# Kernel tuning notes

Measured on AMD Instinct MI355X. Metric: run time of the kernel, lower is better.

Reference implementation:

```python
import jax, jax.numpy as jnp
import numpy as np

N, F, H, R, B, L, C, E, NB = 8192, 512, 256, 16, 32, 256, 7, 262144, 30
D = F + H


def setup_inputs() -> dict:
    ks = jax.random.split(jax.random.key(0), 16)
    g = lambda k, shape, fan: jax.random.normal(k, shape, jnp.float32) / np.sqrt(fan)
    return {
        "x": jax.random.normal(ks[0], (N, F), jnp.float32),
        "edge_index": jax.random.randint(ks[1], (2, E), 0, N),
        "edge_norm": jax.random.uniform(ks[2], (E,), jnp.float32),
        "edge_type": jax.random.randint(ks[3], (E,), 0, R),
        "seq_lengths": jnp.full((B,), L, dtype=jnp.int32),
        "umask": jnp.ones((B, L), jnp.float32),
        "nodal_attn": 1,
        "avec": 0,
        "basis": g(ks[4], (NB, F, H), F),
        "comp": g(ks[5], (R, NB), NB),
        "root1": g(ks[6], (F, H), F),
        "bias1": jnp.zeros((H,), jnp.float32),
        "w_rel": g(ks[7], (H, H), H),
        "b_rel": jnp.zeros((H,), jnp.float32),
        "w_root": g(ks[8], (H, H), H),
        "w_att": g(ks[9], (D, D), D),
        "b_att": jnp.zeros((D,), jnp.float32),
        "w_lin": g(ks[10], (D, H), D),
        "b_lin": jnp.zeros((H,), jnp.float32),
        "w_fc": g(ks[11], (H, C), H),
        "b_fc": jnp.zeros((C,), jnp.float32),
    }


def reference(x, edge_index, edge_norm, edge_type, seq_lengths, umask,
              nodal_attn, avec, basis, comp, root1, bias1, w_rel, b_rel,
              w_root, w_att, b_att, w_lin, b_lin, w_fc, b_fc):
    n = x.shape[0]
    r = comp.shape[0]
    src, dst = edge_index[0], edge_index[1]
    # ---- RGCNConv (num_bases basis decomposition, mean aggregation per relation, root + bias)
    W = jnp.einsum('rb,bfh->rfh', comp, basis)             # [R,F,H]
    xw = jnp.einsum('nf,rfh->nrh', x, W)                   # [N,R,H]
    msg = xw[src, edge_type]                               # [E,H] gather per edge
    seg = dst * r + edge_type                              # per (node, relation) segment
    cnt = jax.ops.segment_sum(jnp.ones((msg.shape[0],), msg.dtype), seg, num_segments=n * r)
    msg = msg / jnp.maximum(cnt[seg], 1.0)[:, None]
    out1 = jax.ops.segment_sum(msg, dst, num_segments=n) + x @ root1 + bias1
    # ---- GraphConv (add aggregation): W_rel * sum_j h_j + b_rel + W_root * h_i
    agg2 = jax.ops.segment_sum(out1[src], dst, num_segments=n)
    out2 = agg2 @ w_rel + b_rel + out1 @ w_root
    emotions = jnp.concatenate([x, out2], axis=-1)          # [N, F+H]
    if int(nodal_attn):
        seq = np.asarray(seq_lengths)                       # static conversation lengths
        starts = np.concatenate([[0], np.cumsum(seq)[:-1]])
        lmax = int(seq.max())
        rows = [jnp.pad(jax.lax.dynamic_slice_in_dim(emotions, int(s), int(l)),
                        ((0, lmax - int(l)), (0, 0)))
                for s, l in zip(starts, seq)]
        M = jnp.stack(rows, 0).transpose(1, 0, 2)           # [L, B, D]
        mask = umask                                        # [B, L]
        # MatchingAttention 'general2', vectorized over all timesteps t
        X = M @ w_att + b_att                               # transform(x_t) for every t: [L,B,D]
        Mm = M * mask.T[:, :, None]                         # mask memory over seq dim
        scores = jnp.einsum('tbd,sbd->tbs', X, Mm) * mask[None]
        a = jax.nn.softmax(jnp.tanh(scores), axis=-1) * mask[None]
        a = a / jnp.sum(a, axis=-1, keepdims=True)
        att = jnp.einsum('tbs,sbd->tbd', a, M)              # [L,B,D]
        hidden = jax.nn.relu(att @ w_lin + b_lin)
    else:
        hidden = jax.nn.relu(emotions @ w_lin + b_lin)
    # dropout is identity in eval mode
    logits = hidden @ w_fc + b_fc
    if int(avec):
        return logits
    return jax.nn.log_softmax(logits, axis=1)  # faithful: torch uses dim=1
```

## Files before the change

kernel.cpp:

```cpp
#include <hip/hip_runtime.h>
#include <hip/hip_bf16.h>

#define NN 8192
#define FF 512
#define HH 256
#define RR 16
#define BB 32
#define LL 256
#define CC 7
#define EE 262144
#define NBASE 30
#define DD 768

constexpr int FLAG_BIAS = 1, FLAG_RELU = 4, FLAG_TANH = 8,
              FLAG_SPLITOUT = 16, FLAG_TAILOUT = 32, FLAG_TAIL2 = 64;

typedef __attribute__((ext_vector_type(8))) short bf16x8;
typedef __attribute__((ext_vector_type(4))) float f32x4;

__global__ __launch_bounds__(256) void detect_dtype(const unsigned short* __restrict__ xs,
                                                    int* __restrict__ flag) {
  __shared__ int red[256];
  int cnt = 0;
  for (int i = threadIdx.x * 2; i < 8192; i += 512) {
    unsigned short u = xs[i];
    int e = (u >> 7) & 0xFF;
    if (e >= 0xC0) cnt++;
  }
  red[threadIdx.x] = cnt;
  __syncthreads();
  for (int s = 128; s > 0; s >>= 1) {
    if (threadIdx.x < s) red[threadIdx.x] += red[threadIdx.x + s];
    __syncthreads();
  }
  if (threadIdx.x == 0) flag[0] = (red[0] > 16) ? 1 : 0;
}

struct PSeg {
  const void* src;
  float* dst;
  __hip_bfloat16* hi;
  __hip_bfloat16* lo;
  __hip_bfloat16* hi2;
  __hip_bfloat16* lo2;
  long n;
  int R, C, ld, off;
  int type;
  int zero;
};
struct PTable {
  PSeg seg[16];
  int count;
  long total;
};

__global__ __launch_bounds__(256) void prep_all(PTable t, const int* __restrict__ flag) {
  const int fp32 = flag[0];
  for (long i = (long)blockIdx.x * 256 + threadIdx.x; i < t.total;
       i += (long)gridDim.x * 256) {
    long off = i;
    int s = 0;
    while (off >= t.seg[s].n) { off -= t.seg[s].n; s++; }
    const PSeg& sg = t.seg[s];
    if (sg.type == 0) {
      float v = 0.f;
      if (!sg.zero)
        v = fp32 ? ((const float*)sg.src)[off]
                 : __bfloat162float(((const __hip_bfloat16*)sg.src)[off]);
      if (sg.dst) sg.dst[off] = v;
      if (sg.hi) {
        __hip_bfloat16 h = __float2bfloat16(v);
        __hip_bfloat16 l = __float2bfloat16(v - __bfloat162float(h));
        sg.hi[off] = h;
        sg.lo[off] = l;
        if (sg.hi2) {
          long d2 = (off >> 9) * DD + (off & 511);
          sg.hi2[d2] = h;
          sg.lo2[d2] = l;
        }
      }
    } else {
      int r = (int)(off % sg.R), c = (int)(off / sg.R);
      float v = fp32 ? ((const float*)sg.src)[(long)r * sg.C + c]
                     : __bfloat162float(((const __hip_bfloat16*)sg.src)[(long)r * sg.C + c]);
      __hip_bfloat16 h = __float2bfloat16(v);
      long d = (long)c * sg.ld + sg.off + r;
      sg.hi[d] = h;
      sg.lo[d] = __float2bfloat16(v - __bfloat162float(h));
    }
  }
}

__global__ __launch_bounds__(256) void wt_gemm(
    const float* __restrict__ basis, const float* __restrict__ comp,
    float* __restrict__ wt_nat) {
  __shared__ float cs[RR * NBASE];
  int tid = threadIdx.x;
  for (int i = tid; i < RR * NBASE; i += 256) cs[i] = comp[i];
  __syncthreads();
  long col = (long)blockIdx.x * 256 + tid;
  float acc[RR] = {};
  for (int b = 0; b < NBASE; ++b) {
    float v = basis[(long)b * 131072 + col];
#pragma unroll
    for (int r = 0; r < RR; ++r) acc[r] += cs[r * NBASE + b] * v;
  }
#pragma unroll
  for (int r = 0; r < RR; ++r) wt_nat[(long)r * 131072 + col] = acc[r];
}

__global__ __launch_bounds__(256) void wt_transpose(
    const float* __restrict__ wt_nat,
    __hip_bfloat16* __restrict__ hi, __hip_bfloat16* __restrict__ lo) {
  __shared__ float t[32][33];
  const int r = blockIdx.z;
  const int f0 = blockIdx.y * 32, h0 = blockIdx.x * 32;
  const int c = threadIdx.x & 31, rw = threadIdx.x >> 5;
  const float* src = wt_nat + ((long)r * 512 + f0) * 256 + h0;
#pragma unroll
  for (int i = 0; i < 4; ++i)
    t[rw + i * 8][c] = src[(long)(rw + i * 8) * 256 + c];
  __syncthreads();
#pragma unroll
  for (int i = 0; i < 4; ++i) {
    int hh = rw + i * 8;
    float v = t[c][hh];
    long orow = (long)(r * 256 + h0 + hh) * 512 + f0 + c;
    __hip_bfloat16 hv = __float2bfloat16(v);
    hi[orow] = hv;
    lo[orow] = __float2bfloat16(v - __bfloat162float(hv));
  }
}

__device__ __forceinline__ void gload_lds16(const void* g, void* l) {
  __builtin_amdgcn_global_load_lds(
      (const __attribute__((address_space(1))) unsigned int*)g,
      (__attribute__((address_space(3))) unsigned int*)l, 16, 0, 0);
}

__global__ __launch_bounds__(256, 3) void mfma_dual(
    const __hip_bfloat16* __restrict__ A, const __hip_bfloat16* __restrict__ Alo,
    const __hip_bfloat16* __restrict__ Bt, const __hip_bfloat16* __restrict__ Btlo,
    const float* __restrict__ bias, float* __restrict__ C, float* __restrict__ Ct,
    __hip_bfloat16* __restrict__ Chi, __hip_bfloat16* __restrict__ Clo,
    __hip_bfloat16* __restrict__ Chi2, __hip_bfloat16* __restrict__ Clo2,
    int K, int ldc, long sA, long sB, long sC, int flags) {
  __shared__ __hip_bfloat16 Ah[128 * 32];
  __shared__ __hip_bfloat16 Bh[128 * 32];
  __shared__ __hip_bfloat16 Al[128 * 32];
  __shared__ __hip_bfloat16 Bl[128 * 32];
  const int tid = threadIdx.x;
  const int w = tid >> 6, lane = tid & 63;
  const long z = blockIdx.z;
  const long row0 = (long)blockIdx.y * 128, col0 = (long)blockIdx.x * 128;
  const int wm = w & 1, wn = w >> 1;
  const int srow0 = (w * 128 + lane) >> 2;
  const int srow1 = (w * 128 + 64 + lane) >> 2;
  const int kch = (lane & 3) * 8;
  const int fr = lane & 15, q = lane >> 4;
  const bool hasAlo = (Alo != nullptr);
  const __hip_bfloat16* Az = A + z * sA;
  const __hip_bfloat16* Alz = hasAlo ? (Alo + z * sA) : nullptr;
  const __hip_bfloat16* Bz = Bt + z * sB;
  const __hip_bfloat16* Blz = Btlo + z * sB;
  const long aoff0 = (row0 + srow0) * K + kch, aoff1 = (row0 + srow1) * K + kch;
  const long boff0 = (col0 + srow0) * K + kch, boff1 = (col0 + srow1) * K + kch;
  f32x4 acc[4][4] = {};
  for (int k0 = 0; k0 < K; k0 += 32) {
    gload_lds16(Az + aoff0 + k0, Ah + w * 1024);
    gload_lds16(Az + aoff1 + k0, Ah + w * 1024 + 512);
    gload_lds16(Bz + boff0 + k0, Bh + w * 1024);
    gload_lds16(Bz + boff1 + k0, Bh + w * 1024 + 512);
    gload_lds16(Blz + boff0 + k0, Bl + w * 1024);
    gload_lds16(Blz + boff1 + k0, Bl + w * 1024 + 512);
    if (hasAlo) {
      gload_lds16(Alz + aoff0 + k0, Al + w * 1024);
      gload_lds16(Alz + aoff1 + k0, Al + w * 1024 + 512);
    }
    __syncthreads();
    bf16x8 ah[4], bh[4], bl[4];
#pragma unroll
    for (int i = 0; i < 4; ++i) {
      ah[i] = *(const bf16x8*)&Ah[(wm * 64 + i * 16 + fr) * 32 + q * 8];
      bh[i] = *(const bf16x8*)&Bh[(wn * 64 + i * 16 + fr) * 32 + q * 8];
      bl[i] = *(const bf16x8*)&Bl[(wn * 64 + i * 16 + fr) * 32 + q * 8];
    }
#pragma unroll
    for (int i = 0; i < 4; ++i)
#pragma unroll
      for (int j = 0; j < 4; ++j) {
        acc[i][j] = __builtin_amdgcn_mfma_f32_16x16x32_bf16(ah[i], bh[j], acc[i][j], 0, 0, 0);
        acc[i][j] = __builtin_amdgcn_mfma_f32_16x16x32_bf16(ah[i], bl[j], acc[i][j], 0, 0, 0);
      }
    if (hasAlo) {
      bf16x8 al[4];
#pragma unroll
      for (int i = 0; i < 4; ++i)
        al[i] = *(const bf16x8*)&Al[(wm * 64 + i * 16 + fr) * 32 + q * 8];
#pragma unroll
      for (int i = 0; i < 4; ++i)
#pragma unroll
        for (int j = 0; j < 4; ++j)
          acc[i][j] = __builtin_amdgcn_mfma_f32_16x16x32_bf16(al[i], bh[j], acc[i][j], 0, 0, 0);
    }
    __syncthreads();
  }
  const int cr = (lane >> 4) * 4, cc = lane & 15;
  float* Cz = C ? (C + z * sC) : nullptr;
  __hip_bfloat16* Chz = Chi ? (Chi + z * sC) : nullptr;
  __hip_bfloat16* Clz = Clo ? (Clo + z * sC) : nullptr;
#pragma unroll
  for (int i = 0; i < 4; ++i) {
    long rbase = row0 + wm * 64 + i * 16 + cr;
#pragma unroll
    for (int j = 0; j < 4; ++j) {
      long col = col0 + wn * 64 + j * 16 + cc;
      float bv = (flags & FLAG_BIAS) ? bias[col] : 0.f;
#pragma unroll
      for (int r = 0; r < 4; ++r) {
        float v = acc[i][j][r] + bv;
        if (flags & FLAG_RELU) v = fmaxf(v, 0.f);
        if (flags & FLAG_TANH) v = tanhf(v);
        long row = rbase + r;
        if ((flags & FLAG_TAIL2) && col >= 768) {
          long off2 = (row >> 8) * 65536 + (col - 768) * 256 + (row & 255);
          __hip_bfloat16 hv = __float2bfloat16(v);
          Chi2[off2] = hv;
          Clo2[off2] = __float2bfloat16(v - __bfloat162float(hv));
        } else if (flags & FLAG_SPLITOUT) {
          long off = row * ldc + col;
          __hip_bfloat16 hv = __float2bfloat16(v);
          Chz[off] = hv;
          Clz[off] = __float2bfloat16(v - __bfloat162float(hv));
        } else if ((flags & FLAG_TAILOUT) && col >= 4096) {
          Ct[row * 256 + (col - 4096)] = v;
        } else {
          Cz[row * ldc + col] = v;
        }
      }
    }
  }
}

__global__ __launch_bounds__(256) void count_edges(
    const int* __restrict__ ei, const int* __restrict__ et, float* __restrict__ cnt) {
  int e = blockIdx.x * 256 + threadIdx.x;
  if (e < EE) atomicAdd(&cnt[ei[EE + e] * RR + et[e]], 1.0f);
}

__global__ __launch_bounds__(256) void scan_rowptr(
    const float* __restrict__ cntf, int* __restrict__ rowptr, int* __restrict__ fill) {
  __shared__ int part[256];
  int tid = threadIdx.x;
  int base = tid * 32;
  int local[32];
  int s = 0;
  for (int i = 0; i < 32; ++i) {
    local[i] = s;
    const float* c = &cntf[(base + i) * RR];
    int d = 0;
#pragma unroll
    for (int r = 0; r < RR; ++r) d += (int)c[r];
    s += d;
  }
  part[tid] = s;
  __syncthreads();
  for (int off = 1; off < 256; off <<= 1) {
    int v = (tid >= off) ? part[tid - off] : 0;
    __syncthreads();
    part[tid] += v;
    __syncthreads();
  }
  int prev = (tid == 0) ? 0 : part[tid - 1];
  for (int i = 0; i < 32; ++i) rowptr[base + i] = prev + local[i];
  if (tid == 255) rowptr[8192] = part[255];
  for (int i = tid; i < 8192; i += 256) fill[i] = 0;
}

__global__ __launch_bounds__(256) void edge_fill(
    const int* __restrict__ ei, const int* __restrict__ et,
    const int* __restrict__ rowptr, int* __restrict__ fill, int* __restrict__ eidx) {
  int e = blockIdx.x * 256 + threadIdx.x;
  if (e < EE) {
    int dst = ei[EE + e];
    int pos = rowptr[dst] + atomicAdd(&fill[dst], 1);
    eidx[pos] = ei[e] | (et[e] << 16);
  }
}

__global__ __launch_bounds__(256) void rgcn_gather(
    const int* __restrict__ rowptr, const int* __restrict__ eidx,
    const float* __restrict__ cntf, const float* __restrict__ xw,
    float* __restrict__ out1, __hip_bfloat16* __restrict__ a2o1_hi,
    __hip_bfloat16* __restrict__ a2o1_lo) {
  const int dst = blockIdx.x;
  const int h = threadIdx.x;
  __shared__ float inv[RR];
  __shared__ int se[256];
  if (h < RR) inv[h] = 1.0f / fmaxf(cntf[dst * RR + h], 1.0f);
  const int beg = rowptr[dst], end = rowptr[dst + 1];
  float a0 = 0.f, a1 = 0.f, a2 = 0.f, a3 = 0.f;
  for (int c0 = beg; c0 < end; c0 += 256) {
    int n = min(256, end - c0);
    __syncthreads();
    if (h < n) se[h] = eidx[c0 + h];
    __syncthreads();
    int i = 0;
    for (; i + 4 <= n; i += 4) {
      int p0 = se[i], p1 = se[i + 1], p2 = se[i + 2], p3 = se[i + 3];
      float v0 = xw[((long)(p0 & 0xFFFF) << 12) + ((p0 >> 16) << 8) + h];
      float v1 = xw[((long)(p1 & 0xFFFF) << 12) + ((p1 >> 16) << 8) + h];
      float v2 = xw[((long)(p2 & 0xFFFF) << 12) + ((p2 >> 16) << 8) + h];
      float v3 = xw[((long)(p3 & 0xFFFF) << 12) + ((p3 >> 16) << 8) + h];
      a0 += v0 * inv[p0 >> 16];
      a1 += v1 * inv[p1 >> 16];
      a2 += v2 * inv[p2 >> 16];
      a3 += v3 * inv[p3 >> 16];
    }
    for (; i < n; ++i) {
      int pk = se[i];
      a0 += xw[((long)(pk & 0xFFFF) << 12) + ((pk >> 16) << 8) + h] * inv[pk >> 16];
    }
  }
  float tot = out1[((long)dst << 8) + h] + ((a0 + a1) + (a2 + a3));
  out1[((long)dst << 8) + h] = tot;
  __hip_bfloat16 hv = __float2bfloat16(tot);
  long d = (long)dst * 512 + 256 + h;
  a2o1_hi[d] = hv;
  a2o1_lo[d] = __float2bfloat16(tot - __bfloat162float(hv));
}

__global__ __launch_bounds__(256) void graphconv_gather(
    const int* __restrict__ rowptr, const int* __restrict__ eidx,
    const float* __restrict__ out1, __hip_bfloat16* __restrict__ a2o1_hi,
    __hip_bfloat16* __restrict__ a2o1_lo) {
  const int dst = blockIdx.x;
  const int h = threadIdx.x;
  __shared__ int se[256];
  const int beg = rowptr[dst], end = rowptr[dst + 1];
  float a0 = 0.f, a1 = 0.f, a2 = 0.f, a3 = 0.f;
  for (int c0 = beg; c0 < end; c0 += 256) {
    int n = min(256, end - c0);
    __syncthreads();
    if (h < n) se[h] = eidx[c0 + h];
    __syncthreads();
    int i = 0;
    for (; i + 4 <= n; i += 4) {
      a0 += out1[((long)(se[i] & 0xFFFF) << 8) + h];
      a1 += out1[((long)(se[i + 1] & 0xFFFF) << 8) + h];
      a2 += out1[((long)(se[i + 2] & 0xFFFF) << 8) + h];
      a3 += out1[((long)(se[i + 3] & 0xFFFF) << 8) + h];
    }
    for (; i < n; ++i) a0 += out1[((long)(se[i] & 0xFFFF) << 8) + h];
  }
  float acc = (a0 + a1) + (a2 + a3);
  __hip_bfloat16 hv = __float2bfloat16(acc);
  long d = (long)dst * 512 + h;
  a2o1_hi[d] = hv;
  a2o1_lo[d] = __float2bfloat16(acc - __bfloat162float(hv));
}

__global__ __launch_bounds__(256) void softmax256(const float* __restrict__ S,
                                                  __hip_bfloat16* __restrict__ Ab) {
  __shared__ float red[256];
  long row = blockIdx.x;
  const float* p = S + row * 256;
  int t = threadIdx.x;
  float v = p[t];
  red[t] = v;
  __syncthreads();
  for (int s = 128; s > 0; s >>= 1) {
    if (t < s) red[t] = fmaxf(red[t], red[t + s]);
    __syncthreads();
  }
  float m = red[0];
  __syncthreads();
  float e = __expf(v - m);
  red[t] = e;
  __syncthreads();
  for (int s = 128; s > 0; s >>= 1) {
    if (t < s) red[t] += red[t + s];
    __syncthreads();
  }
  Ab[row * 256 + t] = __float2bfloat16(e / red[0]);
}

__global__ __launch_bounds__(256) void logits_lsm(
    const float* __restrict__ hidden, const float* __restrict__ w_fc,
    const float* __restrict__ b_fc, void* __restrict__ out_v,
    const int* __restrict__ flag) {
  __shared__ float wf[256 * 7];
  __shared__ float lg[224];
  __shared__ float corr[7];
  int t = blockIdx.x;
  int tid = threadIdx.x;
  for (int i = tid; i < 256 * 7; i += 256) wf[i] = w_fc[i];
  __syncthreads();
  if (tid < 224) {
    int b = tid / 7, c = tid % 7;
    const float* hr = hidden + ((long)((b << 8) + t) << 8);
    float s = b_fc[c];
    for (int k = 0; k < 256; ++k) s += hr[k] * wf[k * 7 + c];
    lg[tid] = s;
  }
  __syncthreads();
  if (tid < 7) {
    float m = -1e30f;
    for (int b = 0; b < BB; ++b) m = fmaxf(m, lg[b * 7 + tid]);
    float sum = 0.f;
    for (int b = 0; b < BB; ++b) sum += __expf(lg[b * 7 + tid] - m);
    corr[tid] = m + logf(sum);
  }
  __syncthreads();
  if (tid < 224) {
    float v = lg[tid] - corr[tid % 7];
    if (flag[0]) ((float*)out_v)[t * 224 + tid] = v;
    else ((__hip_bfloat16*)out_v)[t * 224 + tid] = __float2bfloat16(v);
  }
}

extern "C" void kernel_launch(void* const* d_in, const int* in_sizes, int n_in,
                              void* d_out, int out_size, void* d_ws, size_t ws_size,
                              hipStream_t stream) {
  const int* ei = (const int*)d_in[1];
  const int* et = (const int*)d_in[3];

  float* ws = (float*)d_ws;
  int* flag = (int*)d_ws;
  float* p = ws + 16;
  auto alloc = [&](long nf) { float* r = p; p += nf; return r; };
  float* w_fc_f = alloc(1792);
  float* b_rel_f = alloc(256);
  float* biasx = alloc(4352);
  float* battx = alloc(1024);
  float* b_lin_f = alloc(256);
  float* b_fc_f = alloc(16);
  __hip_bfloat16* x_hi = (__hip_bfloat16*)alloc(2097152);
  __hip_bfloat16* x_lo = (__hip_bfloat16*)alloc(2097152);
  __hip_bfloat16* wae_hi = (__hip_bfloat16*)alloc(393216);
  __hip_bfloat16* wae_lo = (__hip_bfloat16*)alloc(393216);
  __hip_bfloat16* wrr_hi = (__hip_bfloat16*)alloc(65536);
  __hip_bfloat16* wrr_lo = (__hip_bfloat16*)alloc(65536);
  __hip_bfloat16* wtc_hi = (__hip_bfloat16*)alloc(1114112);
  __hip_bfloat16* wtc_lo = (__hip_bfloat16*)alloc(1114112);
  float* basis_f = alloc(3932160);
  float* comp_f = alloc(512);
  float* xw = alloc(33554432);
  float* cnt = alloc(131072);
  float* out1 = alloc(2097152);
  __hip_bfloat16* a2o1_hi = (__hip_bfloat16*)alloc(2097152);
  __hip_bfloat16* a2o1_lo = (__hip_bfloat16*)alloc(2097152);
  float* hidden = alloc(2097152);
  int* rowptr = (int*)alloc(8208);
  int* fillc = (int*)alloc(8192);
  int* eidx = (int*)alloc(262144);
  float* wt_nat = xw;
  float* em = xw;
  __hip_bfloat16* emwT_hi = (__hip_bfloat16*)(em + 2097152);
  __hip_bfloat16* emwT_lo = (__hip_bfloat16*)(em + 3145728);
  __hip_bfloat16* em_hi = (__hip_bfloat16*)(em + 6291456);
  __hip_bfloat16* em_lo = (__hip_bfloat16*)(em + 9437184);
  __hip_bfloat16* X_hi = (__hip_bfloat16*)(em + 12582912);
  __hip_bfloat16* X_lo = (__hip_bfloat16*)(em + 15728640);
  float* scores = em + 18874368;
  __hip_bfloat16* a_b16 = (__hip_bfloat16*)(em + 20971520);

  detect_dtype<<<1, 256, 0, stream>>>((const unsigned short*)d_in[0], flag);
  PTable T{};
  long tot = 0;
  int ns = 0;
  auto segL = [&](const void* s, float* d, __hip_bfloat16* hi, __hip_bfloat16* lo,
                  __hip_bfloat16* hi2, __hip_bfloat16* lo2, long n, int z) {
    T.seg[ns] = PSeg{s, d, hi, lo, hi2, lo2, n, 0, 0, 0, 0, 0, z};
    ns++; tot += n;
  };
  auto segT = [&](const void* s, __hip_bfloat16* hi, __hip_bfloat16* lo,
                  int R, int C, int ld, int off) {
    T.seg[ns] = PSeg{s, nullptr, hi, lo, nullptr, nullptr, (long)R * C, R, C, ld, off, 1, 0};
    ns++; tot += (long)R * C;
  };
  segL(d_in[0], nullptr, x_hi, x_lo, nullptr, nullptr, NN * FF, 0);
  segL(d_in[8], basis_f, nullptr, nullptr, nullptr, nullptr, NBASE * FF * HH, 0);
  segL(d_in[9], comp_f, nullptr, nullptr, nullptr, nullptr, RR * NBASE, 0);
  segL(d_in[13], b_rel_f, nullptr, nullptr, nullptr, nullptr, HH, 0);
  segL(d_in[16], battx, nullptr, nullptr, nullptr, nullptr, DD, 0);
  segL(nullptr, battx + DD, nullptr, nullptr, nullptr, nullptr, 256, 1);
  segL(d_in[18], b_lin_f, nullptr, nullptr, nullptr, nullptr, HH, 0);
  segL(d_in[19], w_fc_f, nullptr, nullptr, nullptr, nullptr, HH * CC, 0);
  segL(d_in[20], b_fc_f, nullptr, nullptr, nullptr, nullptr, CC, 0);
  segL(nullptr, biasx, nullptr, nullptr, nullptr, nullptr, 4096, 1);
  segL(d_in[11], biasx + 4096, nullptr, nullptr, nullptr, nullptr, HH, 0);
  segT(d_in[15], wae_hi, wae_lo, DD, DD, DD, 0);
  segT(d_in[17], wae_hi + 768 * 768, wae_lo + 768 * 768, DD, HH, DD, 0);
  segT(d_in[10], wtc_hi + 4096 * 512, wtc_lo + 4096 * 512, FF, HH, FF, 0);
  segT(d_in[12], wrr_hi, wrr_lo, HH, HH, 512, 0);
  segT(d_in[14], wrr_hi, wrr_lo, HH, HH, 512, 256);
  T.count = ns;
  T.total = tot;
  prep_all<<<4096, 256, 0, stream>>>(T, flag);

  wt_gemm<<<131072 / 256, 256, 0, stream>>>(basis_f, comp_f, wt_nat);
  wt_transpose<<<dim3(8, 16, 16), 256, 0, stream>>>(wt_nat, wtc_hi, wtc_lo);
  mfma_dual<<<dim3(34, 64, 1), 256, 0, stream>>>(
      x_hi, x_lo, wtc_hi, wtc_lo, biasx, xw, out1, nullptr, nullptr, nullptr, nullptr,
      FF, 4096, 0, 0, 0, FLAG_BIAS | FLAG_TAILOUT);
  hipMemsetAsync(cnt, 0, 131072 * sizeof(float), stream);
  count_edges<<<EE / 256, 256, 0, stream>>>(ei, et, cnt);
  scan_rowptr<<<1, 256, 0, stream>>>(cnt, rowptr, fillc);
  edge_fill<<<EE / 256, 256, 0, stream>>>(ei, et, rowptr, fillc, eidx);
  rgcn_gather<<<NN, 256, 0, stream>>>(rowptr, eidx, cnt, xw, out1, a2o1_hi, a2o1_lo);
  graphconv_gather<<<NN, 256, 0, stream>>>(rowptr, eidx, out1, a2o1_hi, a2o1_lo);
  {
    PTable T2{};
    T2.seg[0] = PSeg{nullptr, nullptr, nullptr, nullptr, nullptr, nullptr,
                     (long)NN * FF, 0, 0, 0, 0, 2, 0};
  }
  {
    struct { const __hip_bfloat16 *xh, *xl; __hip_bfloat16 *eh, *el; } args{x_hi, x_lo, em_hi, em_lo};
  }
  extern __global__ void copy_xsplit_k(const __hip_bfloat16*, const __hip_bfloat16*,
                                       __hip_bfloat16*, __hip_bfloat16*);
  copy_xsplit_k<<<(NN * FF) / 256, 256, 0, stream>>>(x_hi, x_lo, em_hi, em_lo);
  mfma_dual<<<dim3(2, 64, 1), 256, 0, stream>>>(
      a2o1_hi, a2o1_lo, wrr_hi, wrr_lo, b_rel_f, nullptr, nullptr,
      em_hi + 512, em_lo + 512, nullptr, nullptr, 512, DD, 0, 0, 0,
      FLAG_BIAS | FLAG_SPLITOUT);
  mfma_dual<<<dim3(8, 64, 1), 256, 0, stream>>>(
      em_hi, em_lo, wae_hi, wae_lo, battx, nullptr, nullptr, X_hi, X_lo,
      emwT_hi, emwT_lo, DD, DD, 0, 0, 0, FLAG_BIAS | FLAG_SPLITOUT | FLAG_TAIL2);
  mfma_dual<<<dim3(2, 2, BB), 256, 0, stream>>>(
      X_hi, X_lo, em_hi, em_lo, nullptr, scores, nullptr, nullptr, nullptr,
      nullptr, nullptr, DD, LL, (long)LL * DD, (long)LL * DD, (long)LL * LL, FLAG_TANH);
  softmax256<<<BB * LL, 256, 0, stream>>>(scores, a_b16);
  mfma_dual<<<dim3(2, 2, BB), 256, 0, stream>>>(
      a_b16, nullptr, emwT_hi, emwT_lo, b_lin_f, hidden, nullptr, nullptr, nullptr,
      nullptr, nullptr, LL, HH, (long)LL * LL, (long)LL * HH, (long)LL * HH,
      FLAG_BIAS | FLAG_RELU);
  logits_lsm<<<LL, 256, 0, stream>>>(hidden, w_fc_f, b_fc_f, d_out, flag);
}

__global__ __launch_bounds__(256) void copy_xsplit_k(
    const __hip_bfloat16* __restrict__ xh, const __hip_bfloat16* __restrict__ xl,
    __hip_bfloat16* __restrict__ eh, __hip_bfloat16* __restrict__ el) {
  int idx = blockIdx.x * 256 + threadIdx.x;
  int n = idx >> 9, f = idx & 511;
  long d = (long)n * DD + f;
  eh[d] = xh[idx];
  el[d] = xl[idx];
}
```

Before: 622.7 us.

## Fuse attention score GEMM with tanh-softmax into one kernel; fold cnt memset into prep

Replaces the batched score GEMM plus the separate fp32 scores buffer and row softmax kernel with one kernel. Each block computes a 128x256 tile of scores with split-bf16 MFMA, applies tanh and exp, reduces row sums through shuffles and shared memory, and writes normalized bf16 attention weights. Because tanh bounds the scores, the max-subtraction pass is dropped. The kernel also zeroes the edge count buffer inside the existing prep pass instead of a separate memset. The fused kernel launches only 64 blocks, each with a large accumulator, so parallelism and occupancy are reduced in exchange for removing the scores round trip.

```diff
diff --git a/kernel.cpp b/kernel.cpp
--- a/kernel.cpp
+++ b/kernel.cpp
@@ -12,7 +12,7 @@
 #define NBASE 30
 #define DD 768
 
-constexpr int FLAG_BIAS = 1, FLAG_RELU = 4, FLAG_TANH = 8,
+constexpr int FLAG_BIAS = 1, FLAG_RELU = 4,
               FLAG_SPLITOUT = 16, FLAG_TAILOUT = 32, FLAG_TAIL2 = 64;
 
 typedef __attribute__((ext_vector_type(8))) short bf16x8;
@@ -41,15 +41,13 @@
   float* dst;
   __hip_bfloat16* hi;
   __hip_bfloat16* lo;
-  __hip_bfloat16* hi2;
-  __hip_bfloat16* lo2;
   long n;
   int R, C, ld, off;
   int type;
   int zero;
 };
 struct PTable {
-  PSeg seg[16];
+  PSeg seg[18];
   int count;
   long total;
 };
@@ -70,14 +68,8 @@
       if (sg.dst) sg.dst[off] = v;
       if (sg.hi) {
         __hip_bfloat16 h = __float2bfloat16(v);
-        __hip_bfloat16 l = __float2bfloat16(v - __bfloat162float(h));
         sg.hi[off] = h;
-        sg.lo[off] = l;
-        if (sg.hi2) {
-          long d2 = (off >> 9) * DD + (off & 511);
-          sg.hi2[d2] = h;
-          sg.lo2[d2] = l;
-        }
+        sg.lo[off] = __float2bfloat16(v - __bfloat162float(h));
       }
     } else {
       int r = (int)(off % sg.R), c = (int)(off / sg.R);
@@ -89,6 +81,16 @@
       sg.lo[d] = __float2bfloat16(v - __bfloat162float(h));
     }
   }
+}
+
+__global__ __launch_bounds__(256) void copy_xsplit_k(
+    const __hip_bfloat16* __restrict__ xh, const __hip_bfloat16* __restrict__ xl,
+    __hip_bfloat16* __restrict__ eh, __hip_bfloat16* __restrict__ el) {
+  int idx = blockIdx.x * 256 + threadIdx.x;
+  int n = idx >> 9, f = idx & 511;
+  long d = (long)n * DD + f;
+  eh[d] = xh[idx];
+  el[d] = xl[idx];
 }
 
 __global__ __launch_bounds__(256) void wt_gemm(
@@ -220,7 +222,6 @@
       for (int r = 0; r < 4; ++r) {
         float v = acc[i][j][r] + bv;
         if (flags & FLAG_RELU) v = fmaxf(v, 0.f);
-        if (flags & FLAG_TANH) v = tanhf(v);
         long row = rbase + r;
         if ((flags & FLAG_TAIL2) && col >= 768) {
           long off2 = (row >> 8) * 65536 + (col - 768) * 256 + (row & 255);
@@ -242,6 +243,95 @@
   }
 }
 
+__global__ __launch_bounds__(256) void score_softmax(
+    const __hip_bfloat16* __restrict__ Xh, const __hip_bfloat16* __restrict__ Xl,
+    const __hip_bfloat16* __restrict__ Eh, const __hip_bfloat16* __restrict__ El,
+    __hip_bfloat16* __restrict__ Ab) {
+  __shared__ __hip_bfloat16 AhS[128 * 32];
+  __shared__ __hip_bfloat16 AlS[128 * 32];
+  __shared__ __hip_bfloat16 BhS[256 * 32];
+  __shared__ __hip_bfloat16 BlS[256 * 32];
+  __shared__ float rsum[128][2];
+  const int tid = threadIdx.x;
+  const int w = tid >> 6, lane = tid & 63;
+  const long z = blockIdx.z;
+  const long row0 = (long)blockIdx.y * 128;
+  const int wm = w & 1, wn = w >> 1;
+  const int kch = (lane & 3) * 8;
+  const int fr = lane & 15, q = lane >> 4;
+  const __hip_bfloat16* Axh = Xh + z * (LL * DD);
+  const __hip_bfloat16* Axl = Xl + z * (LL * DD);
+  const __hip_bfloat16* Beh = Eh + z * (LL * DD);
+  const __hip_bfloat16* Bel = El + z * (LL * DD);
+  const int sa0 = w * 32 + (lane >> 2), sa1 = sa0 + 16;
+  const int sb0 = w * 64 + (lane >> 2);
+  f32x4 acc[4][8] = {};
+  for (int k0 = 0; k0 < DD; k0 += 32) {
+    gload_lds16(Axh + (row0 + sa0) * DD + kch + k0, AhS + w * 1024);
+    gload_lds16(Axh + (row0 + sa1) * DD + kch + k0, AhS + w * 1024 + 512);
+    gload_lds16(Axl + (row0 + sa0) * DD + kch + k0, AlS + w * 1024);
+    gload_lds16(Axl + (row0 + sa1) * DD + kch + k0, AlS + w * 1024 + 512);
+#pragma unroll
+    for (int b = 0; b < 4; ++b) {
+      gload_lds16(Beh + (sb0 + b * 16) * DD + kch + k0, BhS + w * 2048 + b * 512);
+      gload_lds16(Bel + (sb0 + b * 16) * DD + kch + k0, BlS + w * 2048 + b * 512);
+    }
+    __syncthreads();
+    bf16x8 ah[4], al[4];
+#pragma unroll
+    for (int i = 0; i < 4; ++i) {
+      ah[i] = *(const bf16x8*)&AhS[(wm * 64 + i * 16 + fr) * 32 + q * 8];
+      al[i] = *(const bf16x8*)&AlS[(wm * 64 + i * 16 + fr) * 32 + q * 8];
+    }
+#pragma unroll
+    for (int j = 0; j < 8; ++j) {
+      bf16x8 bh = *(const bf16x8*)&BhS[(wn * 128 + j * 16 + fr) * 32 + q * 8];
+      bf16x8 bl = *(const bf16x8*)&BlS[(wn * 128 + j * 16 + fr) * 32 + q * 8];
+#pragma unroll
+      for (int i = 0; i < 4; ++i) {
+        acc[i][j] = __builtin_amdgcn_mfma_f32_16x16x32_bf16(ah[i], bh, acc[i][j], 0, 0, 0);
+        acc[i][j] = __builtin_amdgcn_mfma_f32_16x16x32_bf16(ah[i], bl, acc[i][j], 0, 0, 0);
+        acc[i][j] = __builtin_amdgcn_mfma_f32_16x16x32_bf16(al[i], bh, acc[i][j], 0, 0, 0);
+      }
+    }
+    __syncthreads();
+  }
+  const int cc = lane & 15;
+#pragma unroll
+  for (int i = 0; i < 4; ++i) {
+#pragma unroll
+    for (int rr = 0; rr < 4; ++rr) {
+      float s = 0.f;
+#pragma unroll
+      for (int j = 0; j < 8; ++j) {
+        float e = __expf(tanhf(acc[i][j][rr]));
+        acc[i][j][rr] = e;
+        s += e;
+      }
+      s += __shfl_xor(s, 1);
+      s += __shfl_xor(s, 2);
+      s += __shfl_xor(s, 4);
+      s += __shfl_xor(s, 8);
+      if (cc == 0) rsum[wm * 64 + i * 16 + q * 4 + rr][wn] = s;
+    }
+  }
+  __syncthreads();
+  __hip_bfloat16* Az = Ab + z * 65536;
+#pragma unroll
+  for (int i = 0; i < 4; ++i) {
+#pragma unroll
+    for (int rr = 0; rr < 4; ++rr) {
+      int rloc = wm * 64 + i * 16 + q * 4 + rr;
+      float S = rsum[rloc][0] + rsum[rloc][1];
+      float invS = 1.0f / S;
+      long rb = (row0 + rloc) * 256;
+#pragma unroll
+      for (int j = 0; j < 8; ++j)
+        Az[rb + wn * 128 + j * 16 + cc] = __float2bfloat16(acc[i][j][rr] * invS);
+    }
+  }
+}
+
 __global__ __launch_bounds__(256) void count_edges(
     const int* __restrict__ ei, const int* __restrict__ et, float* __restrict__ cnt) {
   int e = blockIdx.x * 256 + threadIdx.x;
@@ -358,31 +448,6 @@
   long d = (long)dst * 512 + h;
   a2o1_hi[d] = hv;
   a2o1_lo[d] = __float2bfloat16(acc - __bfloat162float(hv));
-}
-
-__global__ __launch_bounds__(256) void softmax256(const float* __restrict__ S,
-                                                  __hip_bfloat16* __restrict__ Ab) {
-  __shared__ float red[256];
-  long row = blockIdx.x;
-  const float* p = S + row * 256;
-  int t = threadIdx.x;
-  float v = p[t];
-  red[t] = v;
-  __syncthreads();
-  for (int s = 128; s > 0; s >>= 1) {
-    if (t < s) red[t] = fmaxf(red[t], red[t + s]);
-    __syncthreads();
-  }
-  float m = red[0];
-  __syncthreads();
-  float e = __expf(v - m);
-  red[t] = e;
-  __syncthreads();
-  for (int s = 128; s > 0; s >>= 1) {
-    if (t < s) red[t] += red[t + s];
-    __syncthreads();
-  }
-  Ab[row * 256 + t] = __float2bfloat16(e / red[0]);
 }
 
 __global__ __launch_bounds__(256) void logits_lsm(
@@ -462,7 +527,6 @@
   __hip_bfloat16* em_lo = (__hip_bfloat16*)(em + 9437184);
   __hip_bfloat16* X_hi = (__hip_bfloat16*)(em + 12582912);
   __hip_bfloat16* X_lo = (__hip_bfloat16*)(em + 15728640);
-  float* scores = em + 18874368;
   __hip_bfloat16* a_b16 = (__hip_bfloat16*)(em + 20971520);
 
   detect_dtype<<<1, 256, 0, stream>>>((const unsigned short*)d_in[0], flag);
@@ -470,26 +534,27 @@
   long tot = 0;
   int ns = 0;
   auto segL = [&](const void* s, float* d, __hip_bfloat16* hi, __hip_bfloat16* lo,
-                  __hip_bfloat16* hi2, __hip_bfloat16* lo2, long n, int z) {
-    T.seg[ns] = PSeg{s, d, hi, lo, hi2, lo2, n, 0, 0, 0, 0, 0, z};
+                  long n, int z) {
+    T.seg[ns] = PSeg{s, d, hi, lo, n, 0, 0, 0, 0, 0, z};
     ns++; tot += n;
   };
   auto segT = [&](const void* s, __hip_bfloat16* hi, __hip_bfloat16* lo,
                   int R, int C, int ld, int off) {
-    T.seg[ns] = PSeg{s, nullptr, hi, lo, nullptr, nullptr, (long)R * C, R, C, ld, off, 1, 0};
+    T.seg[ns] = PSeg{s, nullptr, hi, lo, (long)R * C, R, C, ld, off, 1, 0};
     ns++; tot += (long)R * C;
   };
-  segL(d_in[0], nullptr, x_hi, x_lo, nullptr, nullptr, NN * FF, 0);
-  segL(d_in[8], basis_f, nullptr, nullptr, nullptr, nullptr, NBASE * FF * HH, 0);
-  segL(d_in[9], comp_f, nullptr, nullptr, nullptr, nullptr, RR * NBASE, 0);
-  segL(d_in[13], b_rel_f, nullptr, nullptr, nullptr, nullptr, HH, 0);
-  segL(d_in[16], battx, nullptr, nullptr, nullptr, nullptr, DD, 0);
-  segL(nullptr, battx + DD, nullptr, nullptr, nullptr, nullptr, 256, 1);
-  segL(d_in[18], b_lin_f, nullptr, nullptr, nullptr, nullptr, HH, 0);
-  segL(d_in[19], w_fc_f, nullptr, nullptr, nullptr, nullptr, HH * CC, 0);
-  segL(d_in[20], b_fc_f, nullptr, nullptr, nullptr, nullptr, CC, 0);
-  segL(nullptr, biasx, nullptr, nullptr, nullptr, nullptr, 4096, 1);
-  segL(d_in[11], biasx + 4096, nullptr, nullptr, nullptr, nullptr, HH, 0);
+  segL(d_in[0], nullptr, x_hi, x_lo, NN * FF, 0);
+  segL(d_in[8], basis_f, nullptr, nullptr, NBASE * FF * HH, 0);
+  segL(d_in[9], comp_f, nullptr, nullptr, RR * NBASE, 0);
+  segL(d_in[13], b_rel_f, nullptr, nullptr, HH, 0);
+  segL(d_in[16], battx, nullptr, nullptr, DD, 0);
+  segL(nullptr, battx + DD, nullptr, nullptr, 256, 1);
+  segL(d_in[18], b_lin_f, nullptr, nullptr, HH, 0);
+  segL(d_in[19], w_fc_f, nullptr, nullptr, HH * CC, 0);
+  segL(d_in[20], b_fc_f, nullptr, nullptr, CC, 0);
+  segL(nullptr, biasx, nullptr, nullptr, 4096, 1);
+  segL(d_in[11], biasx + 4096, nullptr, nullptr, HH, 0);
+  segL(nullptr, cnt, nullptr, nullptr, 131072, 1);
   segT(d_in[15], wae_hi, wae_lo, DD, DD, DD, 0);
   segT(d_in[17], wae_hi + 768 * 768, wae_lo + 768 * 768, DD, HH, DD, 0);
   segT(d_in[10], wtc_hi + 4096 * 512, wtc_lo + 4096 * 512, FF, HH, FF, 0);
@@ -504,22 +569,11 @@
   mfma_dual<<<dim3(34, 64, 1), 256, 0, stream>>>(
       x_hi, x_lo, wtc_hi, wtc_lo, biasx, xw, out1, nullptr, nullptr, nullptr, nullptr,
       FF, 4096, 0, 0, 0, FLAG_BIAS | FLAG_TAILOUT);
-  hipMemsetAsync(cnt, 0, 131072 * sizeof(float), stream);
   count_edges<<<EE / 256, 256, 0, stream>>>(ei, et, cnt);
   scan_rowptr<<<1, 256, 0, stream>>>(cnt, rowptr, fillc);
   edge_fill<<<EE / 256, 256, 0, stream>>>(ei, et, rowptr, fillc, eidx);
   rgcn_gather<<<NN, 256, 0, stream>>>(rowptr, eidx, cnt, xw, out1, a2o1_hi, a2o1_lo);
   graphconv_gather<<<NN, 256, 0, stream>>>(rowptr, eidx, out1, a2o1_hi, a2o1_lo);
-  {
-    PTable T2{};
-    T2.seg[0] = PSeg{nullptr, nullptr, nullptr, nullptr, nullptr, nullptr,
-                     (long)NN * FF, 0, 0, 0, 0, 2, 0};
-  }
-  {
-    struct { const __hip_bfloat16 *xh, *xl; __hip_bfloat16 *eh, *el; } args{x_hi, x_lo, em_hi, em_lo};
-  }
-  extern __global__ void copy_xsplit_k(const __hip_bfloat16*, const __hip_bfloat16*,
-                                       __hip_bfloat16*, __hip_bfloat16*);
   copy_xsplit_k<<<(NN * FF) / 256, 256, 0, stream>>>(x_hi, x_lo, em_hi, em_lo);
   mfma_dual<<<dim3(2, 64, 1), 256, 0, stream>>>(
       a2o1_hi, a2o1_lo, wrr_hi, wrr_lo, b_rel_f, nullptr, nullptr,
@@ -528,23 +582,10 @@
   mfma_dual<<<dim3(8, 64, 1), 256, 0, stream>>>(
       em_hi, em_lo, wae_hi, wae_lo, battx, nullptr, nullptr, X_hi, X_lo,
       emwT_hi, emwT_lo, DD, DD, 0, 0, 0, FLAG_BIAS | FLAG_SPLITOUT | FLAG_TAIL2);
-  mfma_dual<<<dim3(2, 2, BB), 256, 0, stream>>>(
-      X_hi, X_lo, em_hi, em_lo, nullptr, scores, nullptr, nullptr, nullptr,
-      nullptr, nullptr, DD, LL, (long)LL * DD, (long)LL * DD, (long)LL * LL, FLAG_TANH);
-  softmax256<<<BB * LL, 256, 0, stream>>>(scores, a_b16);
+  score_softmax<<<dim3(1, 2, BB), 256, 0, stream>>>(X_hi, X_lo, em_hi, em_lo, a_b16);
   mfma_dual<<<dim3(2, 2, BB), 256, 0, stream>>>(
       a_b16, nullptr, emwT_hi, emwT_lo, b_lin_f, hidden, nullptr, nullptr, nullptr,
       nullptr, nullptr, LL, HH, (long)LL * LL, (long)LL * HH, (long)LL * HH,
       FLAG_BIAS | FLAG_RELU);
   logits_lsm<<<LL, 256, 0, stream>>>(hidden, w_fc_f, b_fc_f, d_out, flag);
 }
-
-__global__ __launch_bounds__(256) void copy_xsplit_k(
-    const __hip_bfloat16* __restrict__ xh, const __hip_bfloat16* __restrict__ xl,
-    __hip_bfloat16* __restrict__ eh, __hip_bfloat16* __restrict__ el) {
-  int idx = blockIdx.x * 256 + threadIdx.x;
-  int n = idx >> 9, f = idx & 511;
-  long d = (long)n * DD + f;
-  eh[d] = xh[idx];
-  el[d] = xl[idx];
-}
```

Measured after the change: 633.3 us. Within noise of the previous version (+1.7%).
